# Optimization experiments

Hardware: AMD Instinct MI355X
Metric: run time of the kernel (lower is better)

Reference implementation:

```python
import jax, jax.numpy as jnp
import numpy as np

DIM = 192
HEADS = 4
EPS = 1e-12  # F.normalize default eps


def setup_inputs() -> dict:
    key = jax.random.key(0)
    k0, k1, k2, k3 = jax.random.split(key, 4)
    x = jax.random.normal(k0, (4, DIM, 128, 128), dtype=jnp.float32)
    # qkv 1x1 conv weight: [3*dim, dim, 1, 1] -> stored as [3*dim, dim]
    w_qkv = jax.random.normal(k1, (3 * DIM, DIM), dtype=jnp.float32) * (1.0 / np.sqrt(DIM))
    # depthwise 3x3 conv weight: [3*dim, 1, 3, 3]
    w_dw = jax.random.normal(k2, (3 * DIM, 1, 3, 3), dtype=jnp.float32) * (1.0 / 3.0)
    # project_out 1x1 conv weight: [dim, dim]
    w_proj = jax.random.normal(k3, (DIM, DIM), dtype=jnp.float32) * (1.0 / np.sqrt(DIM))
    # temperature: ones(heads,1,1), requires_grad=False in original
    temperature = jnp.ones((HEADS, 1, 1), dtype=jnp.float32)
    return {"x": x, "w_qkv": w_qkv, "w_dw": w_dw, "w_proj": w_proj,
            "temperature": temperature}


def _l2norm(t):
    # F.normalize(t, dim=-1): t / max(||t||_2, eps)
    n = jnp.sqrt(jnp.sum(t * t, axis=-1, keepdims=True))
    return t / jnp.maximum(n, EPS)


def reference(x, w_qkv, w_dw, w_proj, temperature):
    b, c, h, w = x.shape
    ch = c // HEADS  # channels per head
    # 1x1 conv (no bias) == channel GEMM
    qkv = jnp.einsum('oc,bchw->bohw', w_qkv, x)
    # depthwise 3x3 conv, padding=1, groups=3*dim
    qkv = jax.lax.conv_general_dilated(
        qkv, w_dw, window_strides=(1, 1), padding=((1, 1), (1, 1)),
        dimension_numbers=('NCHW', 'OIHW', 'NCHW'),
        feature_group_count=3 * c)
    q, k, v = jnp.split(qkv, 3, axis=1)
    # b (head ch) h w -> b head ch (h w)
    def rearr(t):
        return t.reshape(b, HEADS, ch, h * w)
    q, k, v = rearr(q), rearr(k), rearr(v)
    q = _l2norm(q)
    k = _l2norm(k)
    # channel-channel attention: [b, head, ch, ch]
    attn = jnp.einsum('bhcn,bhdn->bhcd', q, k) * temperature[None]
    attn = jax.nn.softmax(attn, axis=-1)
    out = jnp.einsum('bhcd,bhdn->bhcn', attn, v)
    out = out.reshape(b, c, h, w)
    out = jnp.einsum('oc,bchw->bohw', w_proj, out)
    return out
```

## Files before the change

### kernel.cpp

```cpp
#include <hip/hip_runtime.h>

typedef unsigned short u16;
typedef float f32x4 __attribute__((ext_vector_type(4)));
typedef __bf16 bf16x8 __attribute__((ext_vector_type(8)));
typedef unsigned short u16x8 __attribute__((ext_vector_type(8)));
typedef unsigned short u16x4 __attribute__((ext_vector_type(4)));

#define DEV static __device__ __forceinline__

DEV u16 f2bf(float f) {
  unsigned int u = __float_as_uint(f);
  u += 0x7FFFu + ((u >> 16) & 1u);
  return (u16)(u >> 16);
}
DEV float bf2f(u16 h) { return __uint_as_float(((unsigned int)h) << 16); }

DEV void gload_lds16(const void* g, void* l) {
  __builtin_amdgcn_global_load_lds(
      (__attribute__((address_space(1))) void*)(unsigned long long)g,
      (__attribute__((address_space(3))) void*)l, 16, 0, 0);
}

DEV void vm_wait(int n) {
  switch (n) {
    case 0:  asm volatile("s_waitcnt vmcnt(0)" ::: "memory"); break;
    case 4:  asm volatile("s_waitcnt vmcnt(4)" ::: "memory"); break;
    case 6:  asm volatile("s_waitcnt vmcnt(6)" ::: "memory"); break;
    case 8:  asm volatile("s_waitcnt vmcnt(8)" ::: "memory"); break;
    case 10: asm volatile("s_waitcnt vmcnt(10)" ::: "memory"); break;
    default: asm volatile("s_waitcnt vmcnt(14)" ::: "memory"); break;
  }
}

__global__ __launch_bounds__(256) void convert_w_kernel(
    const float* __restrict__ in, u16* __restrict__ out, int n) {
  int i = blockIdx.x * 256 + threadIdx.x;
  if (i < n) out[i] = f2bf(in[i]);
}

template <bool IN_F32, bool OUT_BF16, int NJ>
__global__ __launch_bounds__(256, 2) void gemm_bt_kernel(
    const void* __restrict__ Av, const u16* __restrict__ B,
    void* __restrict__ Cv, size_t aBatch, size_t bBatch, size_t cBatch,
    int ldC) {
  __shared__ __align__(16) char smem[73728];
  char* sA = smem;

  const int tid = threadIdx.x, wave = tid >> 6, lane = tid & 63;
  const int id = blockIdx.x;
  const int m0 = (id & 255) * 64, b = id >> 8;
  const char* Bbase = (const char*)(B + (size_t)b * bBatch);

  f32x4 vaf[3][4];
  u16x8 vau[2][4];
  if (IN_F32) {
    const float* Xb = (const float*)Av + (size_t)b * aBatch + m0;
    const int cbl = tid & 15, iq = tid >> 4;
#pragma unroll
    for (int p = 0; p < 3; ++p)
#pragma unroll
      for (int r = 0; r < 4; ++r)
        vaf[p][r] = *(const f32x4*)(Xb + (size_t)((p * 16 + cbl) * 4 + r) *
                                             16384 + iq * 4);
  } else {
    const u16* Vb = (const u16*)Av + (size_t)b * aBatch + m0;
#pragma unroll
    for (int p = 0; p < 2; ++p) {
      const int task = p * 256 + tid;
      if (task < 384) {
        const int cb = task >> 3, io = task & 7;
#pragma unroll
        for (int r = 0; r < 4; ++r)
          vau[p][r] = *(const u16x8*)(Vb + (size_t)(cb * 4 + r) * 16384 +
                                      io * 8);
      }
    }
  }
#pragma unroll
  for (int t = 0; t < 2; ++t) {
    if (t < NJ) {
      const char* Bj = Bbase + (size_t)t * 24576;
      char* sB = smem + 24576 + t * 24576;
#pragma unroll
      for (int i = 0; i < 6; ++i) {
        const int c = i * 4 + wave;
        const int d = c * 1024 + lane * 16;
        const int row = d / 384, inrow = d - row * 384;
        gload_lds16(Bj + row * 384 + (inrow ^ ((row & 7) << 4)), sB + c * 1024);
      }
    }
  }
  if (IN_F32) {
    const int cbl = tid & 15, iq = tid >> 4;
#pragma unroll
    for (int p = 0; p < 3; ++p) {
      const int cb = p * 16 + cbl;
#pragma unroll
      for (int j = 0; j < 4; ++j) {
        const int n = iq * 4 + j;
        u16x4 col;
        col[0] = f2bf(vaf[p][0][j]);
        col[1] = f2bf(vaf[p][1][j]);
        col[2] = f2bf(vaf[p][2][j]);
        col[3] = f2bf(vaf[p][3][j]);
        *(u16x4*)(sA + n * 384 + ((cb * 8) ^ ((n & 7) << 4))) = col;
      }
    }
  } else {
#pragma unroll
    for (int p = 0; p < 2; ++p) {
      const int task = p * 256 + tid;
      if (task < 384) {
        const int cb = task >> 3, io = task & 7;
#pragma unroll
        for (int j = 0; j < 8; ++j) {
          const int n = io * 8 + j;
          u16x4 col;
          col[0] = vau[p][0][j];
          col[1] = vau[p][1][j];
          col[2] = vau[p][2][j];
          col[3] = vau[p][3][j];
          *(u16x4*)(sA + n * 384 + ((cb * 8) ^ ((n & 7) << 4))) = col;
        }
      }
    }
  }
  asm volatile("s_waitcnt lgkmcnt(0)" ::: "memory");
  vm_wait(6);
  __builtin_amdgcn_s_barrier();

  const int wm = wave & 1, wn = wave >> 1;
  const int l15 = lane & 15, lg = lane >> 4;
  const int swm = (l15 & 7) << 4;
  const int rA0 = (wm * 32 + l15) * 384;
  const int rB0 = (wn * 32 + l15) * 384;

  bf16x8 af[2][6];
#pragma unroll
  for (int mi = 0; mi < 2; ++mi)
#pragma unroll
    for (int ks = 0; ks < 6; ++ks)
      af[mi][ks] = *(const bf16x8*)(sA + rA0 + mi * 16 * 384 +
                                    ((ks * 64 + lg * 16) ^ swm));

  f32x4 acc[2][2];
#pragma unroll
  for (int j = 0; j < NJ; ++j) {
    char* sB = smem + 24576 + ((j & 1) ? 24576 : 0);
    bf16x8 bfv[2][6];
#pragma unroll
    for (int nj = 0; nj < 2; ++nj)
#pragma unroll
      for (int ks = 0; ks < 6; ++ks)
        bfv[nj][ks] = *(const bf16x8*)(sB + rB0 + nj * 16 * 384 +
                                       ((ks * 64 + lg * 16) ^ swm));
    asm volatile("s_waitcnt lgkmcnt(0)" ::: "memory");
    __builtin_amdgcn_s_barrier();
    if (j + 2 < NJ) {
      const char* Bj = Bbase + (size_t)(j + 2) * 24576;
#pragma unroll
      for (int i = 0; i < 6; ++i) {
        const int c = i * 4 + wave;
        const int d = c * 1024 + lane * 16;
        const int row = d / 384, inrow = d - row * 384;
        gload_lds16(Bj + row * 384 + (inrow ^ ((row & 7) << 4)), sB + c * 1024);
      }
    }
    if (j > 0) {
      const int j0 = (j - 1) * 64;
      if (OUT_BF16) {
        u16* Cb = (u16*)Cv + (size_t)b * cBatch;
#pragma unroll
        for (int mi = 0; mi < 2; ++mi)
#pragma unroll
          for (int nj = 0; nj < 2; ++nj) {
            u16x4 ov;
#pragma unroll
            for (int r = 0; r < 4; ++r) ov[r] = f2bf(acc[mi][nj][r]);
            *(u16x4*)(Cb + (size_t)(j0 + wn * 32 + nj * 16 + l15) * ldC + m0 +
                      wm * 32 + mi * 16 + lg * 4) = ov;
          }
      } else {
        float* Cb = (float*)Cv + (size_t)b * cBatch;
#pragma unroll
        for (int mi = 0; mi < 2; ++mi)
#pragma unroll
          for (int nj = 0; nj < 2; ++nj)
            *(f32x4*)(Cb + (size_t)(j0 + wn * 32 + nj * 16 + l15) * ldC + m0 +
                      wm * 32 + mi * 16 + lg * 4) = acc[mi][nj];
      }
    }
    __builtin_amdgcn_sched_barrier(0);
#pragma unroll
    for (int mi = 0; mi < 2; ++mi)
#pragma unroll
      for (int nj = 0; nj < 2; ++nj) acc[mi][nj] = (f32x4){0.f, 0.f, 0.f, 0.f};
#pragma unroll
    for (int ks = 0; ks < 6; ++ks)
#pragma unroll
      for (int mi = 0; mi < 2; ++mi)
#pragma unroll
        for (int nj = 0; nj < 2; ++nj)
          acc[mi][nj] = __builtin_amdgcn_mfma_f32_16x16x32_bf16(
              af[mi][ks], bfv[nj][ks], acc[mi][nj], 0, 0, 0);
    if (j + 1 < NJ) {
      vm_wait((j >= 2 ? 4 : 0) + (j + 3 < NJ ? 6 : 0) + (j >= 1 ? 4 : 0));
      __builtin_amdgcn_s_barrier();
    }
  }
  {
    const int j0 = (NJ - 1) * 64;
    if (OUT_BF16) {
      u16* Cb = (u16*)Cv + (size_t)b * cBatch;
#pragma unroll
      for (int mi = 0; mi < 2; ++mi)
#pragma unroll
        for (int nj = 0; nj < 2; ++nj) {
          u16x4 ov;
#pragma unroll
          for (int r = 0; r < 4; ++r) ov[r] = f2bf(acc[mi][nj][r]);
          *(u16x4*)(Cb + (size_t)(j0 + wn * 32 + nj * 16 + l15) * ldC + m0 +
                    wm * 32 + mi * 16 + lg * 4) = ov;
        }
    } else {
      float* Cb = (float*)Cv + (size_t)b * cBatch;
#pragma unroll
      for (int mi = 0; mi < 2; ++mi)
#pragma unroll
        for (int nj = 0; nj < 2; ++nj)
          *(f32x4*)(Cb + (size_t)(j0 + wn * 32 + nj * 16 + l15) * ldC + m0 +
                    wm * 32 + mi * 16 + lg * 4) = acc[mi][nj];
    }
  }
}

__global__ __launch_bounds__(256) void dwconv_kernel(
    u16* __restrict__ qkv, const float* __restrict__ wdw,
    float* __restrict__ sq) {
  __shared__ u16 img[16384];
  __shared__ float red[4];
  const int o = blockIdx.x, b = blockIdx.y;
  const size_t base = ((size_t)b * 576 + o) * 16384;
  const int tid = threadIdx.x, wave = tid >> 6, lane = tid & 63;
#pragma unroll
  for (int i = 0; i < 8; ++i) {
    const int off = (i * 4 + wave) * 1024;
    gload_lds16((const char*)qkv + base * 2 + off + lane * 16, (char*)img + off);
  }
  asm volatile("s_waitcnt vmcnt(0)" ::: "memory");
  __syncthreads();
  float w[9];
#pragma unroll
  for (int j = 0; j < 9; ++j) w[j] = wdw[o * 9 + j];
  float sqacc = 0.f;
  for (int it = 0; it < 8; ++it) {
    const int chunk = it * 256 + tid;
    const int px0 = chunk * 8;
    const int y = px0 >> 7, x0 = px0 & 127;
    float acc[8];
#pragma unroll
    for (int j = 0; j < 8; ++j) acc[j] = 0.f;
#pragma unroll
    for (int dy = -1; dy <= 1; ++dy) {
      const int yy = y + dy;
      float v[10];
      if (yy >= 0 && yy <= 127) {
        const u16* rowp = img + yy * 128 + x0;
        u16x8 m = *(const u16x8*)rowp;
#pragma unroll
        for (int j = 0; j < 8; ++j) v[j + 1] = bf2f(m[j]);
        v[0] = (x0 > 0) ? bf2f(rowp[-1]) : 0.f;
        v[9] = (x0 < 120) ? bf2f(rowp[8]) : 0.f;
      } else {
#pragma unroll
        for (int j = 0; j < 10; ++j) v[j] = 0.f;
      }
      const float w0 = w[(dy + 1) * 3], w1 = w[(dy + 1) * 3 + 1],
                  w2 = w[(dy + 1) * 3 + 2];
#pragma unroll
      for (int j = 0; j < 8; ++j) acc[j] += w0 * v[j] + w1 * v[j + 1] + w2 * v[j + 2];
    }
    u16x8 ov;
#pragma unroll
    for (int j = 0; j < 8; ++j) {
      sqacc += acc[j] * acc[j];
      ov[j] = f2bf(acc[j]);
    }
    *(u16x8*)(qkv + base + px0) = ov;
  }
#pragma unroll
  for (int s = 32; s > 0; s >>= 1) sqacc += __shfl_xor(sqacc, s, 64);
  if (lane == 0) red[wave] = sqacc;
  __syncthreads();
  if (tid == 0) sq[b * 576 + o] = red[0] + red[1] + red[2] + red[3];
}

__global__ __launch_bounds__(256) void gram_kernel(
    const u16* __restrict__ qkv, float* __restrict__ partial) {
  __shared__ u16 tiles[4 * 3072];
  __shared__ float red[4 * 2304];
  const int bh = blockIdx.y, b = bh >> 2, h = bh & 3;
  const int g = blockIdx.x;
  const int wave = threadIdx.x >> 6, lane = threadIdx.x & 63;
  const int n0 = g * 512 + wave * 128;
  const u16* qb = qkv + ((size_t)b * 576 + h * 48) * 16384;
  const u16* kb = qb + (size_t)192 * 16384;
  char* tl = (char*)(tiles + wave * 3072);
  const int l15 = lane & 15, lg = lane >> 4;
  const int swz = (l15 & 3) << 4;
  f32x4 acc[3][3];
#pragma unroll
  for (int i = 0; i < 3; ++i)
#pragma unroll
    for (int j = 0; j < 3; ++j) acc[i][j] = (f32x4){0.f, 0.f, 0.f, 0.f};

  for (int ks = 0; ks < 4; ++ks) {
    const int nn = n0 + ks * 32;
    asm volatile("s_waitcnt lgkmcnt(0)" ::: "memory");
#pragma unroll
    for (int i = 0; i < 6; ++i) {
      const int flat = i * 1024 + lane * 16;
      const int row = flat >> 6, colb = flat & 63;
      const u16* src = (row < 48) ? (qb + (size_t)row * 16384 + nn)
                                  : (kb + (size_t)(row - 48) * 16384 + nn);
      gload_lds16((const char*)src + (colb ^ ((row & 3) << 4)), tl + i * 1024);
    }
    asm volatile("s_waitcnt vmcnt(0)" ::: "memory");
    bf16x8 qf[3], kf[3];
#pragma unroll
    for (int f = 0; f < 3; ++f) {
      qf[f] = *(const bf16x8*)(tl + (f * 16 + l15) * 64 + ((lg * 16) ^ swz));
      kf[f] = *(const bf16x8*)(tl + (48 + f * 16 + l15) * 64 + ((lg * 16) ^ swz));
    }
#pragma unroll
    for (int i = 0; i < 3; ++i)
#pragma unroll
      for (int j = 0; j < 3; ++j)
        acc[i][j] = __builtin_amdgcn_mfma_f32_16x16x32_bf16(qf[i], kf[j],
                                                            acc[i][j], 0, 0, 0);
  }
  {
    float* rw = red + wave * 2304;
#pragma unroll
    for (int i = 0; i < 3; ++i)
#pragma unroll
      for (int j = 0; j < 3; ++j)
#pragma unroll
        for (int r = 0; r < 4; ++r)
          rw[(i * 16 + lg * 4 + r) * 48 + (j * 16 + l15)] = acc[i][j][r];
  }
  __syncthreads();
#pragma unroll
  for (int it = 0; it < 9; ++it) {
    const int p = it * 256 + threadIdx.x;
    const float s = red[p] + red[2304 + p] + red[4608 + p] + red[6912 + p];
    partial[((size_t)bh * 2304 + p) * 32 + g] = s;
  }
}

__global__ __launch_bounds__(256) void reduce_partial_kernel(
    const float* __restrict__ partial, float* __restrict__ G) {
  const int idx = blockIdx.x * 256 + threadIdx.x;
  const f32x4* pp = (const f32x4*)(partial + (size_t)idx * 32);
  const f32x4 a = (pp[0] + pp[1]) + (pp[2] + pp[3]) +
                  (pp[4] + pp[5]) + (pp[6] + pp[7]);
  G[idx] = a.x + a.y + a.z + a.w;
}

__global__ __launch_bounds__(256) void softmax_weff_kernel(
    const float* __restrict__ Gin, const float* __restrict__ sq,
    const float* __restrict__ temp, const float* __restrict__ wproj,
    u16* __restrict__ weff) {
  __shared__ float G[2304];
  __shared__ float wp[192 * 49];
  __shared__ float nq[48], nk[48];
  const int bh = blockIdx.x, b = bh >> 2, h = bh & 3;
  const int tid = threadIdx.x;
#pragma unroll
  for (int it = 0; it < 36; ++it) {
    const int j = it * 256 + tid;
    const int o = j / 48, c = j - o * 48;
    wp[o * 49 + c] = wproj[o * 192 + h * 48 + c];
  }
#pragma unroll
  for (int it = 0; it < 9; ++it) {
    const int p = it * 256 + tid;
    G[p] = Gin[(size_t)bh * 2304 + p];
  }
  if (tid < 48) {
    nq[tid] = fmaxf(sqrtf(sq[b * 576 + h * 48 + tid]), 1e-12f);
    nk[tid] = fmaxf(sqrtf(sq[b * 576 + 192 + h * 48 + tid]), 1e-12f);
  }
  __syncthreads();
  if (tid < 48) {
    const int r = tid;
    const float inq = temp[h] / nq[r];
    float L[48];
    float mx = -3.4e38f;
#pragma unroll 4
    for (int d = 0; d < 48; ++d) {
      const float v = G[r * 48 + d] * inq / nk[d];
      L[d] = v;
      mx = fmaxf(mx, v);
    }
    float s = 0.f;
#pragma unroll 4
    for (int d = 0; d < 48; ++d) {
      const float e = __expf(L[d] - mx);
      L[d] = e;
      s += e;
    }
    const float inv = 1.f / s;
#pragma unroll 4
    for (int d = 0; d < 48; ++d) G[r * 48 + d] = L[d] * inv;
  }
  __syncthreads();
  if (tid < 192) {
    const int o = tid;
    f32x4 acc[12];
#pragma unroll
    for (int dv = 0; dv < 12; ++dv) acc[dv] = (f32x4){0.f, 0.f, 0.f, 0.f};
    for (int c = 0; c < 48; ++c) {
      const float w = wp[o * 49 + c];
      const f32x4* at = (const f32x4*)(G + c * 48);
#pragma unroll
      for (int dv = 0; dv < 12; ++dv) acc[dv] += w * at[dv];
    }
    u16* op = weff + ((size_t)b * 192 + o) * 192 + h * 48;
#pragma unroll
    for (int g8 = 0; g8 < 6; ++g8) {
      u16x8 ov;
#pragma unroll
      for (int j = 0; j < 8; ++j) {
        const int d = g8 * 8 + j;
        ov[j] = f2bf(acc[d >> 2][d & 3]);
      }
      *(u16x8*)(op + g8 * 8) = ov;
    }
  }
}

extern "C" void kernel_launch(void* const* d_in, const int* in_sizes, int n_in,
                              void* d_out, int out_size, void* d_ws,
                              size_t ws_size, hipStream_t stream) {
  (void)in_sizes; (void)n_in; (void)out_size; (void)ws_size;
  const float* x      = (const float*)d_in[0];
  const float* w_qkv  = (const float*)d_in[1];
  const float* w_dw   = (const float*)d_in[2];
  const float* w_proj = (const float*)d_in[3];
  const float* temp   = (const float*)d_in[4];

  char* ws = (char*)d_ws;
  u16*   qkv     = (u16*)ws;
  float* partial = (float*)(ws + 75497472);
  float* G       = (float*)(ws + 80216064);
  float* sq      = (float*)(ws + 80363520);
  u16*   Wq      = (u16*)(ws + 80372736);
  u16*   Weff    = (u16*)(ws + 80593920);

  convert_w_kernel<<<dim3(432), 256, 0, stream>>>(w_qkv, Wq, 110592);
  gemm_bt_kernel<true, true, 9><<<dim3(1024), 256, 0, stream>>>(
      x, Wq, qkv, (size_t)192 * 16384, 0, (size_t)576 * 16384, 16384);
  dwconv_kernel<<<dim3(576, 4), 256, 0, stream>>>(qkv, w_dw, sq);
  gram_kernel<<<dim3(32, 16), 256, 0, stream>>>(qkv, partial);
  reduce_partial_kernel<<<dim3(144), 256, 0, stream>>>(partial, G);
  softmax_weff_kernel<<<dim3(16), 256, 0, stream>>>(G, sq, temp, w_proj, Weff);
  gemm_bt_kernel<false, false, 3><<<dim3(1024), 256, 0, stream>>>(
      qkv + (size_t)384 * 16384, Weff, d_out, (size_t)576 * 16384,
      (size_t)192 * 192, (size_t)192 * 16384, 16384);
}
```

Measured before the change: 135.1 us.

## Prepack B operands into MFMA fragment order and load directly from global

The weight matrices (converted w_qkv and the fused Weff) are now written in a pre-swizzled MFMA fragment layout, so each lane fetches its B fragments with one coalesced 16-byte global load. The GEMM no longer stages B through LDS with async global_load_lds and a double-buffered vmcnt pipeline, which cuts LDS from 72KB to 24KB and removes several barriers. In exchange, B loads now sit in the critical path of every j iteration with no explicit prefetch, relying on L2 hits and occupancy to hide latency. The launch-bounds occupancy hint is also dropped.

```diff
diff --git a/kernel.cpp b/kernel.cpp
--- a/kernel.cpp
+++ b/kernel.cpp
@@ -21,77 +21,44 @@
       (__attribute__((address_space(3))) void*)l, 16, 0, 0);
 }
 
-DEV void vm_wait(int n) {
-  switch (n) {
-    case 0:  asm volatile("s_waitcnt vmcnt(0)" ::: "memory"); break;
-    case 4:  asm volatile("s_waitcnt vmcnt(4)" ::: "memory"); break;
-    case 6:  asm volatile("s_waitcnt vmcnt(6)" ::: "memory"); break;
-    case 8:  asm volatile("s_waitcnt vmcnt(8)" ::: "memory"); break;
-    case 10: asm volatile("s_waitcnt vmcnt(10)" ::: "memory"); break;
-    default: asm volatile("s_waitcnt vmcnt(14)" ::: "memory"); break;
-  }
-}
-
-__global__ __launch_bounds__(256) void convert_w_kernel(
-    const float* __restrict__ in, u16* __restrict__ out, int n) {
-  int i = blockIdx.x * 256 + threadIdx.x;
-  if (i < n) out[i] = f2bf(in[i]);
+__global__ __launch_bounds__(256) void convert_w_pack_kernel(
+    const float* __restrict__ w, u16* __restrict__ out) {
+  const int t = blockIdx.x * 256 + threadIdx.x;
+  const int lane = t & 63, chunk = t >> 6;
+  const int ks = chunk % 6, r = chunk / 6;
+  const int nj = r & 1, wn = (r >> 1) & 1, j = r >> 2;
+  const int row = j * 64 + wn * 32 + nj * 16 + (lane & 15);
+  const int ke = ks * 32 + (lane >> 4) * 8;
+  const f32x4 a = *(const f32x4*)(w + row * 192 + ke);
+  const f32x4 c = *(const f32x4*)(w + row * 192 + ke + 4);
+  u16x8 o;
+  o[0] = f2bf(a.x); o[1] = f2bf(a.y); o[2] = f2bf(a.z); o[3] = f2bf(a.w);
+  o[4] = f2bf(c.x); o[5] = f2bf(c.y); o[6] = f2bf(c.z); o[7] = f2bf(c.w);
+  *(u16x8*)(out + (size_t)t * 8) = o;
 }
 
 template <bool IN_F32, bool OUT_BF16, int NJ>
-__global__ __launch_bounds__(256, 2) void gemm_bt_kernel(
-    const void* __restrict__ Av, const u16* __restrict__ B,
+__global__ __launch_bounds__(256) void gemm_bt_kernel(
+    const void* __restrict__ Av, const u16* __restrict__ Bpack,
     void* __restrict__ Cv, size_t aBatch, size_t bBatch, size_t cBatch,
     int ldC) {
-  __shared__ __align__(16) char smem[73728];
-  char* sA = smem;
+  __shared__ __align__(16) char sA[24576];
 
   const int tid = threadIdx.x, wave = tid >> 6, lane = tid & 63;
   const int id = blockIdx.x;
   const int m0 = (id & 255) * 64, b = id >> 8;
-  const char* Bbase = (const char*)(B + (size_t)b * bBatch);
-
-  f32x4 vaf[3][4];
-  u16x8 vau[2][4];
+  const u16* Bp = Bpack + (size_t)b * bBatch;
+
   if (IN_F32) {
     const float* Xb = (const float*)Av + (size_t)b * aBatch + m0;
     const int cbl = tid & 15, iq = tid >> 4;
+    f32x4 vaf[3][4];
 #pragma unroll
     for (int p = 0; p < 3; ++p)
 #pragma unroll
       for (int r = 0; r < 4; ++r)
         vaf[p][r] = *(const f32x4*)(Xb + (size_t)((p * 16 + cbl) * 4 + r) *
                                              16384 + iq * 4);
-  } else {
-    const u16* Vb = (const u16*)Av + (size_t)b * aBatch + m0;
-#pragma unroll
-    for (int p = 0; p < 2; ++p) {
-      const int task = p * 256 + tid;
-      if (task < 384) {
-        const int cb = task >> 3, io = task & 7;
-#pragma unroll
-        for (int r = 0; r < 4; ++r)
-          vau[p][r] = *(const u16x8*)(Vb + (size_t)(cb * 4 + r) * 16384 +
-                                      io * 8);
-      }
-    }
-  }
-#pragma unroll
-  for (int t = 0; t < 2; ++t) {
-    if (t < NJ) {
-      const char* Bj = Bbase + (size_t)t * 24576;
-      char* sB = smem + 24576 + t * 24576;
-#pragma unroll
-      for (int i = 0; i < 6; ++i) {
-        const int c = i * 4 + wave;
-        const int d = c * 1024 + lane * 16;
-        const int row = d / 384, inrow = d - row * 384;
-        gload_lds16(Bj + row * 384 + (inrow ^ ((row & 7) << 4)), sB + c * 1024);
-      }
-    }
-  }
-  if (IN_F32) {
-    const int cbl = tid & 15, iq = tid >> 4;
 #pragma unroll
     for (int p = 0; p < 3; ++p) {
       const int cb = p * 16 + cbl;
@@ -107,6 +74,19 @@
       }
     }
   } else {
+    const u16* Vb = (const u16*)Av + (size_t)b * aBatch + m0;
+    u16x8 vau[2][4];
+#pragma unroll
+    for (int p = 0; p < 2; ++p) {
+      const int task = p * 256 + tid;
+      if (task < 384) {
+        const int cb = task >> 3, io = task & 7;
+#pragma unroll
+        for (int r = 0; r < 4; ++r)
+          vau[p][r] = *(const u16x8*)(Vb + (size_t)(cb * 4 + r) * 16384 +
+                                      io * 8);
+      }
+    }
 #pragma unroll
     for (int p = 0; p < 2; ++p) {
       const int task = p * 256 + tid;
@@ -125,15 +105,12 @@
       }
     }
   }
-  asm volatile("s_waitcnt lgkmcnt(0)" ::: "memory");
-  vm_wait(6);
-  __builtin_amdgcn_s_barrier();
+  __syncthreads();
 
   const int wm = wave & 1, wn = wave >> 1;
   const int l15 = lane & 15, lg = lane >> 4;
   const int swm = (l15 & 7) << 4;
   const int rA0 = (wm * 32 + l15) * 384;
-  const int rB0 = (wn * 32 + l15) * 384;
 
   bf16x8 af[2][6];
 #pragma unroll
@@ -143,54 +120,16 @@
       af[mi][ks] = *(const bf16x8*)(sA + rA0 + mi * 16 * 384 +
                                     ((ks * 64 + lg * 16) ^ swm));
 
-  f32x4 acc[2][2];
 #pragma unroll
   for (int j = 0; j < NJ; ++j) {
-    char* sB = smem + 24576 + ((j & 1) ? 24576 : 0);
     bf16x8 bfv[2][6];
 #pragma unroll
     for (int nj = 0; nj < 2; ++nj)
 #pragma unroll
       for (int ks = 0; ks < 6; ++ks)
-        bfv[nj][ks] = *(const bf16x8*)(sB + rB0 + nj * 16 * 384 +
-                                       ((ks * 64 + lg * 16) ^ swm));
-    asm volatile("s_waitcnt lgkmcnt(0)" ::: "memory");
-    __builtin_amdgcn_s_barrier();
-    if (j + 2 < NJ) {
-      const char* Bj = Bbase + (size_t)(j + 2) * 24576;
-#pragma unroll
-      for (int i = 0; i < 6; ++i) {
-        const int c = i * 4 + wave;
-        const int d = c * 1024 + lane * 16;
-        const int row = d / 384, inrow = d - row * 384;
-        gload_lds16(Bj + row * 384 + (inrow ^ ((row & 7) << 4)), sB + c * 1024);
-      }
-    }
-    if (j > 0) {
-      const int j0 = (j - 1) * 64;
-      if (OUT_BF16) {
-        u16* Cb = (u16*)Cv + (size_t)b * cBatch;
-#pragma unroll
-        for (int mi = 0; mi < 2; ++mi)
-#pragma unroll
-          for (int nj = 0; nj < 2; ++nj) {
-            u16x4 ov;
-#pragma unroll
-            for (int r = 0; r < 4; ++r) ov[r] = f2bf(acc[mi][nj][r]);
-            *(u16x4*)(Cb + (size_t)(j0 + wn * 32 + nj * 16 + l15) * ldC + m0 +
-                      wm * 32 + mi * 16 + lg * 4) = ov;
-          }
-      } else {
-        float* Cb = (float*)Cv + (size_t)b * cBatch;
-#pragma unroll
-        for (int mi = 0; mi < 2; ++mi)
-#pragma unroll
-          for (int nj = 0; nj < 2; ++nj)
-            *(f32x4*)(Cb + (size_t)(j0 + wn * 32 + nj * 16 + l15) * ldC + m0 +
-                      wm * 32 + mi * 16 + lg * 4) = acc[mi][nj];
-      }
-    }
-    __builtin_amdgcn_sched_barrier(0);
+        bfv[nj][ks] = *(const bf16x8*)(
+            Bp + ((size_t)((j * 4 + wn * 2 + nj) * 6 + ks) * 512) + lane * 8);
+    f32x4 acc[2][2];
 #pragma unroll
     for (int mi = 0; mi < 2; ++mi)
 #pragma unroll
@@ -203,13 +142,7 @@
         for (int nj = 0; nj < 2; ++nj)
           acc[mi][nj] = __builtin_amdgcn_mfma_f32_16x16x32_bf16(
               af[mi][ks], bfv[nj][ks], acc[mi][nj], 0, 0, 0);
-    if (j + 1 < NJ) {
-      vm_wait((j >= 2 ? 4 : 0) + (j + 3 < NJ ? 6 : 0) + (j >= 1 ? 4 : 0));
-      __builtin_amdgcn_s_barrier();
-    }
-  }
-  {
-    const int j0 = (NJ - 1) * 64;
+    const int j0 = j * 64;
     if (OUT_BF16) {
       u16* Cb = (u16*)Cv + (size_t)b * cBatch;
 #pragma unroll
@@ -426,16 +359,20 @@
 #pragma unroll
       for (int dv = 0; dv < 12; ++dv) acc[dv] += w * at[dv];
     }
-    u16* op = weff + ((size_t)b * 192 + o) * 192 + h * 48;
+    u16* op = weff + (size_t)b * 36864;
+    const int jj = o >> 6, wn = (o >> 5) & 1, nj = (o >> 4) & 1, l15 = o & 15;
 #pragma unroll
     for (int g8 = 0; g8 < 6; ++g8) {
+      const int c2 = h * 48 + g8 * 8;
+      const int ks = c2 >> 5, lg = (c2 >> 3) & 3;
       u16x8 ov;
 #pragma unroll
-      for (int j = 0; j < 8; ++j) {
-        const int d = g8 * 8 + j;
-        ov[j] = f2bf(acc[d >> 2][d & 3]);
+      for (int q = 0; q < 8; ++q) {
+        const int d = g8 * 8 + q;
+        ov[q] = f2bf(acc[d >> 2][d & 3]);
       }
-      *(u16x8*)(op + g8 * 8) = ov;
+      *(u16x8*)(op + ((size_t)((jj * 4 + wn * 2 + nj) * 6 + ks) * 512) +
+                (lg * 16 + l15) * 8) = ov;
     }
   }
 }
@@ -458,7 +395,7 @@
   u16*   Wq      = (u16*)(ws + 80372736);
   u16*   Weff    = (u16*)(ws + 80593920);
 
-  convert_w_kernel<<<dim3(432), 256, 0, stream>>>(w_qkv, Wq, 110592);
+  convert_w_pack_kernel<<<dim3(54), 256, 0, stream>>>(w_qkv, Wq);
   gemm_bt_kernel<true, true, 9><<<dim3(1024), 256, 0, stream>>>(
       x, Wq, qkv, (size_t)192 * 16384, 0, (size_t)576 * 16384, 16384);
   dwconv_kernel<<<dim3(576, 4), 256, 0, stream>>>(qkv, w_dw, sq);
@@ -467,5 +404,5 @@
   softmax_weff_kernel<<<dim3(16), 256, 0, stream>>>(G, sq, temp, w_proj, Weff);
   gemm_bt_kernel<false, false, 3><<<dim3(1024), 256, 0, stream>>>(
       qkv + (size_t)384 * 16384, Weff, d_out, (size_t)576 * 16384,
-      (size_t)192 * 192, (size_t)192 * 16384, 16384);
-}
+      (size_t)36864, (size_t)192 * 16384, 16384);
+}
```

Result: slower. 141.4 us (+4.7%).

## Give each wave its own B slice to drop block barriers in GEMM loop

Applied to the files above, without the earlier changes.

The 1x1-conv GEMM kernel now splits output rows across waves: each wave owns a contiguous range of 16-row B tiles, loads them into its own double-buffered LDS region, and computes a full 64-column M tile per step. Previously all four waves shared 64x64 B tiles and needed block-wide barriers every iteration. Per-wave vmcnt waits replace those barriers, and each wave now holds all A fragments (4x6), which increases register use. The grid becomes 2D (256,4) instead of decoding the batch from a flat index.

```diff
diff --git a/kernel.cpp b/kernel.cpp
--- a/kernel.cpp
+++ b/kernel.cpp
@@ -38,7 +38,7 @@
   if (i < n) out[i] = f2bf(in[i]);
 }
 
-template <bool IN_F32, bool OUT_BF16, int NJ>
+template <bool IN_F32, bool OUT_BF16, int NJT>
 __global__ __launch_bounds__(256, 2) void gemm_bt_kernel(
     const void* __restrict__ Av, const u16* __restrict__ B,
     void* __restrict__ Cv, size_t aBatch, size_t bBatch, size_t cBatch,
@@ -47,9 +47,10 @@
   char* sA = smem;
 
   const int tid = threadIdx.x, wave = tid >> 6, lane = tid & 63;
-  const int id = blockIdx.x;
-  const int m0 = (id & 255) * 64, b = id >> 8;
+  const int m0 = blockIdx.x * 64, b = blockIdx.y;
   const char* Bbase = (const char*)(B + (size_t)b * bBatch);
+  char* bufs = smem + 24576 + wave * 12288;
+  const int jwbase = wave * (NJT * 16);
 
   f32x4 vaf[3][4];
   u16x8 vau[2][4];
@@ -78,15 +79,14 @@
   }
 #pragma unroll
   for (int t = 0; t < 2; ++t) {
-    if (t < NJ) {
-      const char* Bj = Bbase + (size_t)t * 24576;
-      char* sB = smem + 24576 + t * 24576;
+    if (t < NJT) {
 #pragma unroll
       for (int i = 0; i < 6; ++i) {
-        const int c = i * 4 + wave;
-        const int d = c * 1024 + lane * 16;
+        const int d = i * 1024 + lane * 16;
         const int row = d / 384, inrow = d - row * 384;
-        gload_lds16(Bj + row * 384 + (inrow ^ ((row & 7) << 4)), sB + c * 1024);
+        gload_lds16(Bbase + (size_t)(jwbase + t * 16 + row) * 384 +
+                        (inrow ^ ((row & 7) << 4)),
+                    bufs + t * 6144 + i * 1024);
       }
     }
   }
@@ -126,110 +126,63 @@
     }
   }
   asm volatile("s_waitcnt lgkmcnt(0)" ::: "memory");
-  vm_wait(6);
   __builtin_amdgcn_s_barrier();
 
-  const int wm = wave & 1, wn = wave >> 1;
   const int l15 = lane & 15, lg = lane >> 4;
   const int swm = (l15 & 7) << 4;
-  const int rA0 = (wm * 32 + l15) * 384;
-  const int rB0 = (wn * 32 + l15) * 384;
-
-  bf16x8 af[2][6];
-#pragma unroll
-  for (int mi = 0; mi < 2; ++mi)
+
+  bf16x8 af[4][6];
+#pragma unroll
+  for (int mi = 0; mi < 4; ++mi)
 #pragma unroll
     for (int ks = 0; ks < 6; ++ks)
-      af[mi][ks] = *(const bf16x8*)(sA + rA0 + mi * 16 * 384 +
+      af[mi][ks] = *(const bf16x8*)(sA + (mi * 16 + l15) * 384 +
                                     ((ks * 64 + lg * 16) ^ swm));
 
-  f32x4 acc[2][2];
-#pragma unroll
-  for (int j = 0; j < NJ; ++j) {
-    char* sB = smem + 24576 + ((j & 1) ? 24576 : 0);
-    bf16x8 bfv[2][6];
-#pragma unroll
-    for (int nj = 0; nj < 2; ++nj)
-#pragma unroll
-      for (int ks = 0; ks < 6; ++ks)
-        bfv[nj][ks] = *(const bf16x8*)(sB + rB0 + nj * 16 * 384 +
-                                       ((ks * 64 + lg * 16) ^ swm));
-    asm volatile("s_waitcnt lgkmcnt(0)" ::: "memory");
-    __builtin_amdgcn_s_barrier();
-    if (j + 2 < NJ) {
-      const char* Bj = Bbase + (size_t)(j + 2) * 24576;
-#pragma unroll
-      for (int i = 0; i < 6; ++i) {
-        const int c = i * 4 + wave;
-        const int d = c * 1024 + lane * 16;
-        const int row = d / 384, inrow = d - row * 384;
-        gload_lds16(Bj + row * 384 + (inrow ^ ((row & 7) << 4)), sB + c * 1024);
-      }
-    }
-    if (j > 0) {
-      const int j0 = (j - 1) * 64;
-      if (OUT_BF16) {
-        u16* Cb = (u16*)Cv + (size_t)b * cBatch;
-#pragma unroll
-        for (int mi = 0; mi < 2; ++mi)
-#pragma unroll
-          for (int nj = 0; nj < 2; ++nj) {
-            u16x4 ov;
-#pragma unroll
-            for (int r = 0; r < 4; ++r) ov[r] = f2bf(acc[mi][nj][r]);
-            *(u16x4*)(Cb + (size_t)(j0 + wn * 32 + nj * 16 + l15) * ldC + m0 +
-                      wm * 32 + mi * 16 + lg * 4) = ov;
-          }
-      } else {
-        float* Cb = (float*)Cv + (size_t)b * cBatch;
-#pragma unroll
-        for (int mi = 0; mi < 2; ++mi)
-#pragma unroll
-          for (int nj = 0; nj < 2; ++nj)
-            *(f32x4*)(Cb + (size_t)(j0 + wn * 32 + nj * 16 + l15) * ldC + m0 +
-                      wm * 32 + mi * 16 + lg * 4) = acc[mi][nj];
-      }
-    }
+#pragma unroll
+  for (int t = 0; t < NJT; ++t) {
+    vm_wait(t == 0 ? (NJT > 1 ? 6 : 0) : (4 + (t + 1 < NJT ? 6 : 0)));
     __builtin_amdgcn_sched_barrier(0);
-#pragma unroll
-    for (int mi = 0; mi < 2; ++mi)
-#pragma unroll
-      for (int nj = 0; nj < 2; ++nj) acc[mi][nj] = (f32x4){0.f, 0.f, 0.f, 0.f};
+    char* bw = bufs + (t & 1) * 6144;
+    bf16x8 bfv[6];
 #pragma unroll
     for (int ks = 0; ks < 6; ++ks)
-#pragma unroll
-      for (int mi = 0; mi < 2; ++mi)
-#pragma unroll
-        for (int nj = 0; nj < 2; ++nj)
-          acc[mi][nj] = __builtin_amdgcn_mfma_f32_16x16x32_bf16(
-              af[mi][ks], bfv[nj][ks], acc[mi][nj], 0, 0, 0);
-    if (j + 1 < NJ) {
-      vm_wait((j >= 2 ? 4 : 0) + (j + 3 < NJ ? 6 : 0) + (j >= 1 ? 4 : 0));
-      __builtin_amdgcn_s_barrier();
-    }
-  }
-  {
-    const int j0 = (NJ - 1) * 64;
+      bfv[ks] = *(const bf16x8*)(bw + l15 * 384 + ((ks * 64 + lg * 16) ^ swm));
+    f32x4 acc[4];
+#pragma unroll
+    for (int mi = 0; mi < 4; ++mi) acc[mi] = (f32x4){0.f, 0.f, 0.f, 0.f};
+#pragma unroll
+    for (int ks = 0; ks < 6; ++ks)
+#pragma unroll
+      for (int mi = 0; mi < 4; ++mi)
+        acc[mi] = __builtin_amdgcn_mfma_f32_16x16x32_bf16(af[mi][ks], bfv[ks],
+                                                          acc[mi], 0, 0, 0);
+    const int jrow = jwbase + t * 16 + l15;
     if (OUT_BF16) {
       u16* Cb = (u16*)Cv + (size_t)b * cBatch;
 #pragma unroll
-      for (int mi = 0; mi < 2; ++mi)
-#pragma unroll
-        for (int nj = 0; nj < 2; ++nj) {
-          u16x4 ov;
-#pragma unroll
-          for (int r = 0; r < 4; ++r) ov[r] = f2bf(acc[mi][nj][r]);
-          *(u16x4*)(Cb + (size_t)(j0 + wn * 32 + nj * 16 + l15) * ldC + m0 +
-                    wm * 32 + mi * 16 + lg * 4) = ov;
-        }
+      for (int mi = 0; mi < 4; ++mi) {
+        u16x4 ov;
+#pragma unroll
+        for (int r = 0; r < 4; ++r) ov[r] = f2bf(acc[mi][r]);
+        *(u16x4*)(Cb + (size_t)jrow * ldC + m0 + mi * 16 + lg * 4) = ov;
+      }
     } else {
       float* Cb = (float*)Cv + (size_t)b * cBatch;
 #pragma unroll
-      for (int mi = 0; mi < 2; ++mi)
-#pragma unroll
-        for (int nj = 0; nj < 2; ++nj)
-          *(f32x4*)(Cb + (size_t)(j0 + wn * 32 + nj * 16 + l15) * ldC + m0 +
-                    wm * 32 + mi * 16 + lg * 4) = acc[mi][nj];
+      for (int mi = 0; mi < 4; ++mi)
+        *(f32x4*)(Cb + (size_t)jrow * ldC + m0 + mi * 16 + lg * 4) = acc[mi];
+    }
+    if (t + 2 < NJT) {
+      __builtin_amdgcn_sched_barrier(0);
+#pragma unroll
+      for (int i = 0; i < 6; ++i) {
+        const int d = i * 1024 + lane * 16;
+        const int row = d / 384, inrow = d - row * 384;
+        gload_lds16(Bbase + (size_t)(jwbase + (t + 2) * 16 + row) * 384 +
+                        (inrow ^ ((row & 7) << 4)),
+                    bw + i * 1024);
+      }
     }
   }
 }
@@ -459,13 +412,13 @@
   u16*   Weff    = (u16*)(ws + 80593920);
 
   convert_w_kernel<<<dim3(432), 256, 0, stream>>>(w_qkv, Wq, 110592);
-  gemm_bt_kernel<true, true, 9><<<dim3(1024), 256, 0, stream>>>(
+  gemm_bt_kernel<true, true, 9><<<dim3(256, 4), 256, 0, stream>>>(
       x, Wq, qkv, (size_t)192 * 16384, 0, (size_t)576 * 16384, 16384);
   dwconv_kernel<<<dim3(576, 4), 256, 0, stream>>>(qkv, w_dw, sq);
   gram_kernel<<<dim3(32, 16), 256, 0, stream>>>(qkv, partial);
   reduce_partial_kernel<<<dim3(144), 256, 0, stream>>>(partial, G);
   softmax_weff_kernel<<<dim3(16), 256, 0, stream>>>(G, sq, temp, w_proj, Weff);
-  gemm_bt_kernel<false, false, 3><<<dim3(1024), 256, 0, stream>>>(
+  gemm_bt_kernel<false, false, 3><<<dim3(256, 4), 256, 0, stream>>>(
       qkv + (size_t)384 * 16384, Weff, d_out, (size_t)576 * 16384,
       (size_t)192 * 192, (size_t)192 * 16384, 16384);
 }
```

Result: no change. 135.6 us (+0.4%).
